# Performance work log

Measured on AMD Instinct MI355X. Metric: run time of the kernel, lower is better.

Reference implementation:

```python
import jax, jax.numpy as jnp
import numpy as np

NEG = -1e9  # finite stand-in for -inf so grads stay NaN-free
BLANK = 0

def _lse3(a, b, c):
    m = jnp.maximum(jnp.maximum(a, b), c)
    return m + jnp.log(jnp.exp(a - m) + jnp.exp(b - m) + jnp.exp(c - m))

def setup_inputs() -> dict:
    key = jax.random.key(0)
    k1, k2, k3, k4 = jax.random.split(key, 4)
    T, B, C, S = 1024, 128, 256, 128
    logits = jax.random.normal(k1, (T, B, C), dtype=jnp.float32)
    log_probs = jax.nn.log_softmax(logits, axis=-1)  # CTCLoss expects log-probs
    y = jax.random.randint(k2, (B, S), 1, C)                 # labels in [1, C), never blank
    input_lengths = jax.random.randint(k3, (B,), 768, T + 1)  # 768..T
    target_lengths = jax.random.randint(k4, (B,), 64, S + 1)  # 64..S
    return {"log_probs": log_probs, "y": y,
            "input_lengths": input_lengths, "target_lengths": target_lengths}

def _ctc_loss(log_probs, y, input_lengths, target_lengths):
    T, B, C = log_probs.shape
    S = y.shape[1]
    L = 2 * S + 1  # extended label sequence: blank, y1, blank, y2, ..., blank

    ext = jnp.zeros((B, L), dtype=y.dtype).at[:, 1::2].set(y)  # even slots = blank(0)
    pos = jnp.arange(L)
    prev2 = jnp.concatenate([jnp.full((B, 2), BLANK, dtype=ext.dtype), ext[:, :-2]], axis=1)
    allow_skip = (pos[None, :] >= 2) & (ext != BLANK) & (ext != prev2)  # [B, L]

    # init alpha at t=0: only s=0 (blank) and s=1 (first label) reachable
    lp0 = log_probs[0]  # [B, C]
    alpha0 = jnp.full((B, L), NEG, dtype=log_probs.dtype)
    alpha0 = alpha0.at[:, 0].set(lp0[:, BLANK])
    alpha0 = alpha0.at[:, 1].set(jnp.take_along_axis(lp0, ext[:, 1:2], axis=1)[:, 0])

    def step(alpha, xs):
        lp_t, t = xs  # lp_t: [B, C]
        a0 = alpha
        a1 = jnp.concatenate([jnp.full((B, 1), NEG, alpha.dtype), alpha[:, :-1]], axis=1)
        a2 = jnp.concatenate([jnp.full((B, 2), NEG, alpha.dtype), alpha[:, :-2]], axis=1)
        a2 = jnp.where(allow_skip, a2, NEG)
        emit = jnp.take_along_axis(lp_t, ext, axis=1)  # [B, L]
        new = _lse3(a0, a1, a2) + emit
        # freeze alpha for samples whose input has already ended
        new = jnp.where(t < input_lengths[:, None], new, alpha)
        return new, None

    ts = jnp.arange(1, T)
    alpha_T, _ = jax.lax.scan(step, alpha0, (log_probs[1:], ts))

    # final log-likelihood: logsumexp of alpha at positions 2*tl and 2*tl-1
    idx_hi = (2 * target_lengths)[:, None]       # [B,1]
    idx_lo = (2 * target_lengths - 1)[:, None]
    a_hi = jnp.take_along_axis(alpha_T, idx_hi, axis=1)[:, 0]
    a_lo = jnp.take_along_axis(alpha_T, idx_lo, axis=1)[:, 0]
    m = jnp.maximum(a_hi, a_lo)
    ll = m + jnp.log(jnp.exp(a_hi - m) + jnp.exp(a_lo - m))
    loss = -ll  # per-sample negative log-likelihood

    # zero_infinity=True: zero out infeasible (effectively -inf likelihood) samples
    loss = jnp.where(loss < 0.5 * (-NEG), loss, 0.0)

    # reduction='mean': divide each loss by its target length, then batch mean
    return jnp.mean(loss / target_lengths.astype(loss.dtype))

def reference(log_probs, y, input_lengths, target_lengths):
    return _ctc_loss(log_probs, y, input_lengths, target_lengths)
```

## Files before the change

### kernel.cpp

```cpp
#include <hip/hip_runtime.h>


#define PF 8
#define CTC_C 256

__device__ __forceinline__ void renorm(double& Oa, double& Ob, double& Ea,
                                       double& Eb, double& E128, double& logC) {
  double m = fmax(fmax(Oa, Ob), fmax(Ea, Eb));
#pragma unroll
  for (int off = 32; off > 0; off >>= 1)
    m = fmax(m, __shfl_xor(m, off));
  m = fmax(m, E128);
  if (m > 0.) {
    long long bits = __double_as_longlong(m);
    int eb = (int)((bits >> 52) & 0x7ff);
    int e = eb - 1022;
    double s = __longlong_as_double((long long)(2045 - eb) << 52);
    Oa *= s; Ob *= s; Ea *= s; Eb *= s; E128 *= s;
    logC += (double)e * 0.6931471805599453;
  }
}

__global__ __launch_bounds__(64)
void ctc_fwd(const float* __restrict__ lp, const int* __restrict__ y,
             const int* __restrict__ ilen, const int* __restrict__ tlen,
             float* __restrict__ out, int T, int B, int S) {
  const int b = blockIdx.x;
  const int l = threadIdx.x;
  const long rowstride = (long)B * CTC_C;

  const int len = ilen[b];
  const int tl  = tlen[b];

  const int ya = y[(size_t)b * S + 2 * l];
  const int yb = y[(size_t)b * S + 2 * l + 1];
  const int yprev = __shfl_up(yb, 1);
  const bool skipA = (l > 0) && (ya != yprev);
  const bool skipB = (yb != ya);

  const float* row0 = lp + (size_t)b * CTC_C;
  const int y0 = y[(size_t)b * S];
  double Ea = (l == 0) ? (double)__expf(row0[0])  : 0.;
  double Oa = (l == 0) ? (double)__expf(row0[y0]) : 0.;
  double Eb = 0., Ob = 0., E128 = 0.;
  double logC = 0.;

  float pA[PF], pB[PF], pQ[PF];
#pragma unroll
  for (int d = 0; d < PF; ++d) {
    int t = 1 + d; t = (t < T) ? t : (T - 1);
    const float* r = lp + (size_t)t * rowstride + (size_t)b * CTC_C;
    pA[d] = r[ya]; pB[d] = r[yb]; pQ[d] = r[0];
  }

  const int nsteps = len - 1;
  const int nchunks = nsteps / PF;
  int t0 = 1;

  for (int c = 0; c < nchunks; ++c) {
#pragma unroll
    for (int d = 0; d < PF; ++d) {
      const int t = t0 + d;
      double pa = (double)__expf(pA[d]);
      double pb = (double)__expf(pB[d]);
      double pq = (double)__expf(pQ[d]);
      int tn = t + PF; tn = (tn < T) ? tn : (T - 1);
      const float* r = lp + (size_t)tn * rowstride + (size_t)b * CTC_C;
      pA[d] = r[ya]; pB[d] = r[yb]; pQ[d] = r[0];

      double Opm1 = __shfl_up(Ob, 1);
      Opm1 = (l == 0) ? 0. : Opm1;
      double O127 = __shfl(Ob, 63);

      double nOa = (Oa + Ea + (skipA ? Opm1 : 0.)) * pa;
      double nOb = (Ob + Eb + (skipB ? Oa   : 0.)) * pb;
      double nEa = (Ea + Opm1) * pq;
      double nEb = (Eb + Oa) * pq;
      E128 = (E128 + O127) * pq;
      Oa = nOa; Ob = nOb; Ea = nEa; Eb = nEb;

      if ((d & 7) == 7) renorm(Oa, Ob, Ea, Eb, E128, logC);
    }
    t0 += PF;
  }

#pragma unroll
  for (int d = 0; d < PF; ++d) {
    const int t = t0 + d;
    if (t <= nsteps) {
      double pa = (double)__expf(pA[d]);
      double pb = (double)__expf(pB[d]);
      double pq = (double)__expf(pQ[d]);
      double Opm1 = __shfl_up(Ob, 1);
      Opm1 = (l == 0) ? 0. : Opm1;
      double O127 = __shfl(Ob, 63);
      double nOa = (Oa + Ea + (skipA ? Opm1 : 0.)) * pa;
      double nOb = (Ob + Eb + (skipB ? Oa   : 0.)) * pb;
      double nEa = (Ea + Opm1) * pq;
      double nEb = (Eb + Oa) * pq;
      E128 = (E128 + O127) * pq;
      Oa = nOa; Ob = nOb; Ea = nEa; Eb = nEb;
      if ((d & 7) == 7) renorm(Oa, Ob, Ea, Eb, E128, logC);
    }
  }

  double vEa = __shfl(Ea, (tl >> 1) & 63);
  double vEb = __shfl(Eb, (tl >> 1) & 63);
  double vhi = (tl == S) ? E128 : ((tl & 1) ? vEb : vEa);
  int s2 = tl - 1;
  double vOa = __shfl(Oa, (s2 >> 1) & 63);
  double vOb = __shfl(Ob, (s2 >> 1) & 63);
  double vlo = (s2 & 1) ? vOb : vOa;

  double sum = vhi + vlo;
  double loss;
  if (sum > 0.) {
    loss = -(logC + log(sum));
  } else {
    loss = 1e30;
  }
  if (!(loss < 5.0e8)) loss = 0.;
  float contrib = (float)(loss / (double)tl / (double)B);
  if (l == 0) atomicAdd(out, contrib);
}

extern "C" void kernel_launch(void* const* d_in, const int* in_sizes, int n_in,
                              void* d_out, int out_size, void* d_ws, size_t ws_size,
                              hipStream_t stream) {
  const float* lp   = (const float*)d_in[0];
  const int*   yy   = (const int*)d_in[1];
  const int*   ilen = (const int*)d_in[2];
  const int*   tlen = (const int*)d_in[3];
  float* out = (float*)d_out;

  int B = in_sizes[2];
  int S = in_sizes[1] / B;
  int T = in_sizes[0] / (B * CTC_C);

  hipMemsetAsync(out, 0, sizeof(float), stream);
  ctc_fwd<<<B, 64, 0, stream>>>(lp, yy, ilen, tlen, out, T, B, S);
}
```

Before: 299.2 us.

## Use DPP lane shifts and reductions, two-stage exp prefetch pipeline in CTC recursion

The per-step lane shift of Ob now uses a DPP wavefront shift-right instead of `__shfl_up`, and each lane updates E128 locally instead of broadcasting lane 63 with `__shfl`. The renormalisation max becomes an integer max over exponent words, done with DPP row ops plus readlanes instead of a chain of `__shfl_xor`. Loads are prefetched 16 steps ahead and exp'd 8 steps ahead, with 32-bit clamped byte offsets. The goal is to shorten the serial per-timestep dependency chain, which was dominated by LDS-based shuffle latency. The cost is more registers, and the renorm drops its m>0 guard, which changes behaviour only when all values are zero.

```diff
diff --git a/kernel.cpp b/kernel.cpp
--- a/kernel.cpp
+++ b/kernel.cpp
@@ -1,24 +1,48 @@
 #include <hip/hip_runtime.h>
 
 
-#define PF 8
 #define CTC_C 256
+#define NRDY 8
+#define NRAW 16
+
+__device__ __forceinline__ unsigned umin32(unsigned a, unsigned b) { return a < b ? a : b; }
+
+__device__ __forceinline__ double wshr1_f64(double x) {
+  int lo = __double2loint(x), hi = __double2hiint(x);
+  lo = __builtin_amdgcn_update_dpp(0, lo, 0x138, 0xf, 0xf, true);
+  hi = __builtin_amdgcn_update_dpp(0, hi, 0x138, 0xf, 0xf, true);
+  return __hiloint2double(hi, lo);
+}
+
+template <int CTRL>
+__device__ __forceinline__ unsigned dppmax(unsigned v) {
+  unsigned t = (unsigned)__builtin_amdgcn_update_dpp(0, (int)v, CTRL, 0xf, 0xf, true);
+  return v > t ? v : t;
+}
 
 __device__ __forceinline__ void renorm(double& Oa, double& Ob, double& Ea,
                                        double& Eb, double& E128, double& logC) {
-  double m = fmax(fmax(Oa, Ob), fmax(Ea, Eb));
-#pragma unroll
-  for (int off = 32; off > 0; off >>= 1)
-    m = fmax(m, __shfl_xor(m, off));
-  m = fmax(m, E128);
-  if (m > 0.) {
-    long long bits = __double_as_longlong(m);
-    int eb = (int)((bits >> 52) & 0x7ff);
-    int e = eb - 1022;
-    double s = __longlong_as_double((long long)(2045 - eb) << 52);
-    Oa *= s; Ob *= s; Ea *= s; Eb *= s; E128 *= s;
-    logC += (double)e * 0.6931471805599453;
-  }
+  unsigned m =       (unsigned)__double2hiint(Oa);
+  unsigned h;
+  h = (unsigned)__double2hiint(Ob);   m = m > h ? m : h;
+  h = (unsigned)__double2hiint(Ea);   m = m > h ? m : h;
+  h = (unsigned)__double2hiint(Eb);   m = m > h ? m : h;
+  h = (unsigned)__double2hiint(E128); m = m > h ? m : h;
+  m = dppmax<0xB1>(m);
+  m = dppmax<0x4E>(m);
+  m = dppmax<0x141>(m);
+  m = dppmax<0x140>(m);
+  unsigned r0 = (unsigned)__builtin_amdgcn_readlane((int)m, 0);
+  unsigned r1 = (unsigned)__builtin_amdgcn_readlane((int)m, 16);
+  unsigned r2 = (unsigned)__builtin_amdgcn_readlane((int)m, 32);
+  unsigned r3 = (unsigned)__builtin_amdgcn_readlane((int)m, 48);
+  unsigned m01 = r0 > r1 ? r0 : r1;
+  unsigned m23 = r2 > r3 ? r2 : r3;
+  unsigned smax = m01 > m23 ? m01 : m23;
+  int eb = (int)(smax >> 20);
+  double s = __hiloint2double((int)((unsigned)(2045 - eb) << 20), 0);
+  Oa *= s; Ob *= s; Ea *= s; Eb *= s; E128 *= s;
+  logC += (double)(eb - 1022) * 0.6931471805599453;
 }
 
 __global__ __launch_bounds__(64)
@@ -27,7 +51,8 @@
              float* __restrict__ out, int T, int B, int S) {
   const int b = blockIdx.x;
   const int l = threadIdx.x;
-  const long rowstride = (long)B * CTC_C;
+  const size_t rowstrideF = (size_t)B * CTC_C;
+  const unsigned ROWB = (unsigned)(B * CTC_C * 4);
 
   const int len = ilen[b];
   const int tl  = tlen[b];
@@ -42,72 +67,90 @@
   const int y0 = y[(size_t)b * S];
   double Ea = (l == 0) ? (double)__expf(row0[0])  : 0.;
   double Oa = (l == 0) ? (double)__expf(row0[y0]) : 0.;
-  double Eb = 0., Ob = 0., E128 = 0.;
-  double logC = 0.;
+  double Eb = 0., Ob = 0., E128 = 0., logC = 0.;
 
-  float pA[PF], pB[PF], pQ[PF];
+  float  rA[NRAW], rB[NRAW], rQ[NRAW];
+  double eA[NRDY], eB[NRDY], eQ[NRDY];
+
 #pragma unroll
-  for (int d = 0; d < PF; ++d) {
-    int t = 1 + d; t = (t < T) ? t : (T - 1);
-    const float* r = lp + (size_t)t * rowstride + (size_t)b * CTC_C;
-    pA[d] = r[ya]; pB[d] = r[yb]; pQ[d] = r[0];
+  for (int t = 1; t <= NRDY; ++t) {
+    const float* r = lp + (size_t)t * rowstrideF + (size_t)b * CTC_C;
+    eA[t & 7] = (double)__expf(r[ya]);
+    eB[t & 7] = (double)__expf(r[yb]);
+    eQ[t & 7] = (double)__expf(r[0]);
+  }
+#pragma unroll
+  for (int t = NRDY + 1; t <= NRDY + NRAW; ++t) {
+    const float* r = lp + (size_t)t * rowstrideF + (size_t)b * CTC_C;
+    rA[t & 15] = r[ya];
+    rB[t & 15] = r[yb];
+    rQ[t & 15] = r[0];
   }
 
+  const char* base = (const char*)lp;
+  const unsigned rowoff = (unsigned)b * CTC_C * 4u;
+  unsigned offA = (unsigned)(NRDY + NRAW + 1) * ROWB + rowoff + 4u * (unsigned)ya;
+  unsigned offB = (unsigned)(NRDY + NRAW + 1) * ROWB + rowoff + 4u * (unsigned)yb;
+  unsigned offQ = (unsigned)(NRDY + NRAW + 1) * ROWB + rowoff;
+  const unsigned capA = (unsigned)(T - 1) * ROWB + rowoff + 4u * (unsigned)ya;
+  const unsigned capB = (unsigned)(T - 1) * ROWB + rowoff + 4u * (unsigned)yb;
+  const unsigned capQ = (unsigned)(T - 1) * ROWB + rowoff;
+  offA = umin32(offA, capA); offB = umin32(offB, capB); offQ = umin32(offQ, capQ);
+
+#define CTC_STEP(i_)                                                          \
+  do {                                                                        \
+    const int d8  = (1 + (i_)) & 7;                                           \
+    const int d16 = (9 + (i_)) & 15;                                          \
+    const double pa = eA[d8], pb = eB[d8], pq = eQ[d8];                       \
+    eA[d8] = (double)__expf(rA[d16]);                                         \
+    eB[d8] = (double)__expf(rB[d16]);                                         \
+    eQ[d8] = (double)__expf(rQ[d16]);                                         \
+    rA[d16] = *(const float*)(base + offA);                                   \
+    rB[d16] = *(const float*)(base + offB);                                   \
+    rQ[d16] = *(const float*)(base + offQ);                                   \
+    offA = umin32(offA + ROWB, capA);                                         \
+    offB = umin32(offB + ROWB, capB);                                         \
+    offQ = umin32(offQ + ROWB, capQ);                                         \
+    const double Opm1 = wshr1_f64(Ob);              \
+    const double EaOp = Ea + Opm1;                                            \
+    const double EbOa = Eb + Oa;                                              \
+    const double tA = skipA ? EaOp : Ea;                                      \
+    const double tB = skipB ? EbOa : Eb;                                      \
+    const double nOa = (Oa + tA) * pa;                                        \
+    const double nOb = (Ob + tB) * pb;                                        \
+    Ea = EaOp * pq;                                                           \
+    Eb = EbOa * pq;                                                           \
+    E128 = (E128 + Ob) * pq;                        \
+    Oa = nOa; Ob = nOb;                                                       \
+  } while (0)
+
   const int nsteps = len - 1;
-  const int nchunks = nsteps / PF;
-  int t0 = 1;
+  const int nch = nsteps >> 4;
+  const int rem = nsteps & 15;
 
-  for (int c = 0; c < nchunks; ++c) {
+  for (int c = 0; c < nch; ++c) {
 #pragma unroll
-    for (int d = 0; d < PF; ++d) {
-      const int t = t0 + d;
-      double pa = (double)__expf(pA[d]);
-      double pb = (double)__expf(pB[d]);
-      double pq = (double)__expf(pQ[d]);
-      int tn = t + PF; tn = (tn < T) ? tn : (T - 1);
-      const float* r = lp + (size_t)tn * rowstride + (size_t)b * CTC_C;
-      pA[d] = r[ya]; pB[d] = r[yb]; pQ[d] = r[0];
-
-      double Opm1 = __shfl_up(Ob, 1);
-      Opm1 = (l == 0) ? 0. : Opm1;
-      double O127 = __shfl(Ob, 63);
-
-      double nOa = (Oa + Ea + (skipA ? Opm1 : 0.)) * pa;
-      double nOb = (Ob + Eb + (skipB ? Oa   : 0.)) * pb;
-      double nEa = (Ea + Opm1) * pq;
-      double nEb = (Eb + Oa) * pq;
-      E128 = (E128 + O127) * pq;
-      Oa = nOa; Ob = nOb; Ea = nEa; Eb = nEb;
-
-      if ((d & 7) == 7) renorm(Oa, Ob, Ea, Eb, E128, logC);
-    }
-    t0 += PF;
-  }
-
-#pragma unroll
-  for (int d = 0; d < PF; ++d) {
-    const int t = t0 + d;
-    if (t <= nsteps) {
-      double pa = (double)__expf(pA[d]);
-      double pb = (double)__expf(pB[d]);
-      double pq = (double)__expf(pQ[d]);
-      double Opm1 = __shfl_up(Ob, 1);
-      Opm1 = (l == 0) ? 0. : Opm1;
-      double O127 = __shfl(Ob, 63);
-      double nOa = (Oa + Ea + (skipA ? Opm1 : 0.)) * pa;
-      double nOb = (Ob + Eb + (skipB ? Oa   : 0.)) * pb;
-      double nEa = (Ea + Opm1) * pq;
-      double nEb = (Eb + Oa) * pq;
-      E128 = (E128 + O127) * pq;
-      Oa = nOa; Ob = nOb; Ea = nEa; Eb = nEb;
-      if ((d & 7) == 7) renorm(Oa, Ob, Ea, Eb, E128, logC);
+    for (int i = 0; i < 16; ++i) {
+      CTC_STEP(i);
+      if ((i & 7) == 7) renorm(Oa, Ob, Ea, Eb, E128, logC);
     }
   }
+  if (rem) {
+#pragma unroll
+    for (int i = 0; i < 16; ++i) {
+      if (i < rem) {
+        CTC_STEP(i);
+        if ((i & 7) == 7) renorm(Oa, Ob, Ea, Eb, E128, logC);
+      }
+    }
+  }
+#undef CTC_STEP
 
   double vEa = __shfl(Ea, (tl >> 1) & 63);
   double vEb = __shfl(Eb, (tl >> 1) & 63);
-  double vhi = (tl == S) ? E128 : ((tl & 1) ? vEb : vEa);
-  int s2 = tl - 1;
+  double vE128 = __shfl(E128, 63);
+  double vhi = (tl == S) ? vE128 : ((tl & 1) ? vEb : vEa);
+  const int s2 = tl - 1;
   double vOa = __shfl(Oa, (s2 >> 1) & 63);
   double vOb = __shfl(Ob, (s2 >> 1) & 63);
   double vlo = (s2 & 1) ? vOb : vOa;
```

Measured after the change: 276.0 us. 7.7% less time.
